# Optimization experiments

Measured on AMD Instinct MI355X. Metric: run time of the kernel, lower is better.

## Reference

```python
import jax, jax.numpy as jnp
import numpy as np

NUM_HEADS = 16


def setup_inputs() -> dict:
    key = jax.random.key(0)
    ks = jax.random.split(key, 4)
    B, C, T, D = 1, 1, 3072, 1024
    s = 1.0 / np.sqrt(D)
    return {
        "x": jax.random.normal(ks[0], (B, C, T, D), dtype=jnp.float32),
        "Wq": jax.random.normal(ks[1], (D, D), dtype=jnp.float32) * s,
        "bq": jnp.zeros((D,), dtype=jnp.float32),
        "Wk": jax.random.normal(ks[2], (D, D), dtype=jnp.float32) * s,
        "bk": jnp.zeros((D,), dtype=jnp.float32),
        "Wv": jax.random.normal(ks[3], (D, D), dtype=jnp.float32) * s,
        "bv": jnp.zeros((D,), dtype=jnp.float32),
        "gamma": jnp.float32(0.5),  # learned scalar; 0.0 at torch init, nonzero here for a meaningful signal
    }


def reference(x, Wq, bq, Wk, bk, Wv, bv, gamma):
    # x: (B, C, T, D); Linear acts on last dim (torch: y = x @ W.T + b)
    B, C, T, D = x.shape
    H = NUM_HEADS
    q = (jnp.einsum("bctd,ed->bcte", x, Wq) + bq).reshape(B, -1, T, H)  # (B, X, T, H), X = C*D/H
    k = (jnp.einsum("bctd,ed->bcte", x, Wk) + bk).reshape(B, -1, T, H)
    v = (jnp.einsum("bctd,ed->bcte", x, Wv) + bv).reshape(B, -1, T, H)
    q = q.transpose(0, 3, 2, 1)  # (B, H, T, X)
    k = k.transpose(0, 3, 1, 2)  # (B, H, X, T)
    energy = q @ k               # (B, H, T, T)  -- note: NO 1/sqrt(d) scaling, as in source
    attn = jax.nn.softmax(energy, axis=-1)
    v = v.transpose(0, 3, 2, 1)  # (B, H, T, X)
    out = attn @ v               # (B, H, T, X)
    out = out.transpose(0, 2, 3, 1).reshape(B, T, -1)  # (B, T, X*H) = (B, T, C*D)
    # residual broadcast: (B, T, C*D) + (B, C, T, D); valid since B == C == 1
    return gamma * out + x
```

## Files before the change

### kernel.cpp

```cpp
#include <hip/hip_runtime.h>


typedef _Float16 v8h __attribute__((ext_vector_type(8)));
typedef _Float16 v4h __attribute__((ext_vector_type(4)));
typedef float    v4f __attribute__((ext_vector_type(4)));

#define TSEQ 3072
#define DM   1024
#define NH   16
#define XD   64
#define LOG2E 1.44269504f

__device__ __forceinline__ void async_load16(const void* g, void* l) {
  __builtin_amdgcn_global_load_lds(
      (const __attribute__((address_space(1))) unsigned int*)g,
      (__attribute__((address_space(3))) unsigned int*)l,
      16, 0, 0);
}

__device__ __forceinline__ float fexp2(float x) {
  float r; asm("v_exp_f32 %0, %1" : "=v"(r) : "v"(x)); return r;
}

extern "C" __global__ __launch_bounds__(256) void cvt_kernel(
    const float* __restrict__ x, const float* __restrict__ wq,
    const float* __restrict__ wk, const float* __restrict__ wv,
    _Float16* __restrict__ xb, _Float16* __restrict__ wb)
{
  const int NX4 = (TSEQ * DM) / 4;
  const int NT  = NX4 * 2;
  for (int i = blockIdx.x * blockDim.x + threadIdx.x; i < NT;
       i += gridDim.x * blockDim.x) {
    float4 v;
    _Float16* dst;
    if (i < NX4) {
      v = ((const float4*)x)[i];
      dst = xb + (size_t)i * 4;
    } else {
      const int j = i - NX4;
      const int n = j >> 8;
      if (n < 1024)      v = ((const float4*)wq)[j];
      else if (n < 2048) v = ((const float4*)wk)[j - 262144];
      else               v = ((const float4*)wv)[j - 524288];
      dst = wb + (size_t)j * 4;
    }
    v4h h;
    h[0] = (_Float16)v.x; h[1] = (_Float16)v.y;
    h[2] = (_Float16)v.z; h[3] = (_Float16)v.w;
    *(v4h*)dst = h;
  }
}

extern "C" __global__ __launch_bounds__(256) void qkv_gemm_kernel(
    const _Float16* __restrict__ xb, const _Float16* __restrict__ wb,
    const float* __restrict__ bq, const float* __restrict__ bk,
    const float* __restrict__ bv,
    _Float16* __restrict__ qlin, _Float16* __restrict__ klin,
    _Float16* __restrict__ vlin)
{
  __shared__ _Float16 As[128 * 32];
  __shared__ _Float16 Bs[128 * 32];
  const int tid = threadIdx.x;
  const int w = tid >> 6, l = tid & 63;
  const int li = l & 15, lg = l >> 4;
  const int wm = w >> 1, wn = w & 1;
  const int bid = blockIdx.x;
  const int swz = (bid & 7) * 72 + (bid >> 3);
  const int m0 = (swz / 24) * 128, n0 = (swz % 24) * 128;
  v4f acc[4][4] = {};
  const int srow = l >> 2;
  const int scol = (l & 3) * 8;
  for (int k0 = 0; k0 < DM; k0 += 32) {
#pragma unroll
    for (int c = 0; c < 2; ++c) {
      const int rbase = c * 64 + w * 16;
      async_load16(xb + (size_t)(m0 + rbase + srow) * DM + k0 + scol, &As[rbase * 32]);
      async_load16(wb + (size_t)(n0 + rbase + srow) * DM + k0 + scol, &Bs[rbase * 32]);
    }
    __syncthreads();
    v8h af[4], bf[4];
#pragma unroll
    for (int mi = 0; mi < 4; ++mi)
      af[mi] = *(const v8h*)&As[(wm * 64 + mi * 16 + li) * 32 + lg * 8];
#pragma unroll
    for (int ni = 0; ni < 4; ++ni)
      bf[ni] = *(const v8h*)&Bs[(wn * 64 + ni * 16 + li) * 32 + lg * 8];
#pragma unroll
    for (int mi = 0; mi < 4; ++mi)
#pragma unroll
      for (int ni = 0; ni < 4; ++ni)
        acc[mi][ni] = __builtin_amdgcn_mfma_f32_16x16x32_f16(
            af[mi], bf[ni], acc[mi][ni], 0, 0, 0);
    __syncthreads();
  }
  const int which = n0 >> 10;
  const int ebase = n0 & 1023;
  const float* bias = which == 0 ? bq : (which == 1 ? bk : bv);
  _Float16* outp = which == 0 ? qlin : (which == 1 ? klin : vlin);
#pragma unroll
  for (int mi = 0; mi < 4; ++mi)
#pragma unroll
    for (int r = 0; r < 4; ++r) {
      const int t = m0 + wm * 64 + mi * 16 + lg * 4 + r;
#pragma unroll
      for (int ni = 0; ni < 4; ++ni) {
        const int e = ebase + wn * 64 + ni * 16 + li;
        outp[(size_t)t * DM + e] = (_Float16)(acc[mi][ni][r] + bias[e]);
      }
    }
}

extern "C" __global__ __launch_bounds__(256) void repack_kernel(
    const _Float16* __restrict__ qlin, const _Float16* __restrict__ klin,
    const _Float16* __restrict__ vlin,
    _Float16* __restrict__ qh, _Float16* __restrict__ kh,
    _Float16* __restrict__ vt)
{
  const int NE = NH * TSEQ * XD;
  for (int g = blockIdx.x * blockDim.x + threadIdx.x; g < 3 * NE;
       g += gridDim.x * blockDim.x) {
    if (g < 2 * NE) {
      const int gg = (g < NE) ? g : g - NE;
      const int xx = gg & 63;
      const int rest = gg >> 6;
      const int h = rest / TSEQ;
      const int i = rest - h * TSEQ;
      const int t = xx * 48 + (i >> 6);
      const int e = ((i & 63) << 4) + h;
      if (g < NE) qh[gg] = qlin[t * DM + e];
      else        kh[gg] = (_Float16)((float)klin[t * DM + e] * LOG2E);
    } else {
      const int o = g - 2 * NE;
      const int j = o % TSEQ;
      const int rest = o / TSEQ;
      const int xx = rest & 63;
      const int h = rest >> 6;
      const int t = xx * 48 + (j >> 6);
      const int e = ((j & 63) << 4) + h;
      vt[o] = vlin[t * DM + e];
    }
  }
}

extern "C" __global__ __launch_bounds__(256) void attn_kernel(
    const _Float16* __restrict__ qh, const _Float16* __restrict__ kh,
    const _Float16* __restrict__ vt, _Float16* __restrict__ pOut)
{
  __shared__ _Float16 Ks[64 * 64];
  __shared__ _Float16 Vs[64 * 64];
  const int tid = threadIdx.x;
  const int w = tid >> 6, l = tid & 63;
  const int li = l & 15, lg = l >> 4;
  const int head = blockIdx.y;
  const int i0 = blockIdx.x * 64;
  const size_t hb = (size_t)head * TSEQ * XD;

  v8h qf0, qf1;
  {
    const _Float16* qrow = qh + hb + (size_t)(i0 + w * 16 + li) * XD;
    qf0 = *(const v8h*)(qrow + lg * 8);
    qf1 = *(const v8h*)(qrow + 32 + lg * 8);
  }
  float m2 = 24.0f * LOG2E;
  float l4 = 0.0f;
  v4f oacc[4] = {};
  const int r8 = l >> 3, c8 = l & 7;

  for (int j0 = 0; j0 < TSEQ; j0 += 64) {
#pragma unroll
    for (int s = 0; s < 2; ++s) {
      const int n = w * 2 + s;
      const int row = n * 8 + r8;
      async_load16(kh + hb + (size_t)(j0 + row) * XD + ((c8 ^ (row & 7)) * 8),
                   Ks + n * 512);
      async_load16(vt + hb + (size_t)row * TSEQ + j0 + ((c8 ^ (row & 7)) * 8),
                   Vs + n * 512);
    }
    __syncthreads();

    v4f e4[4];
#pragma unroll
    for (int kt = 0; kt < 4; ++kt) {
      const int krow = kt * 16 + li;
      const v8h kf0 = *(const v8h*)&Ks[krow * 64 + ((lg ^ (krow & 7)) * 8)];
      const v8h kf1 = *(const v8h*)&Ks[krow * 64 + (((4 + lg) ^ (krow & 7)) * 8)];
      v4f a = {};
      a = __builtin_amdgcn_mfma_f32_16x16x32_f16(kf0, qf0, a, 0, 0, 0);
      a = __builtin_amdgcn_mfma_f32_16x16x32_f16(kf1, qf1, a, 0, 0, 0);
      e4[kt] = a;
    }

    float p[4][4];
#pragma unroll
    for (int kt = 0; kt < 4; ++kt)
#pragma unroll
      for (int r = 0; r < 4; ++r) p[kt][r] = fexp2(e4[kt][r] - m2);

    float lmax = fmaxf(fmaxf(fmaxf(e4[0][0], e4[0][1]), fmaxf(e4[0][2], e4[0][3])),
                       fmaxf(fmaxf(e4[1][0], e4[1][1]), fmaxf(e4[1][2], e4[1][3])));
    lmax = fmaxf(lmax,
           fmaxf(fmaxf(fmaxf(e4[2][0], e4[2][1]), fmaxf(e4[2][2], e4[2][3])),
                 fmaxf(fmaxf(e4[3][0], e4[3][1]), fmaxf(e4[3][2], e4[3][3]))));
    if (__any(lmax > m2 + 11.5f)) {
      float rm = lmax;
      rm = fmaxf(rm, __shfl_xor(rm, 16, 64));
      rm = fmaxf(rm, __shfl_xor(rm, 32, 64));
      const float fs = (rm > m2) ? fexp2(m2 - rm) : 1.0f;
#pragma unroll
      for (int kt = 0; kt < 4; ++kt)
#pragma unroll
        for (int r = 0; r < 4; ++r) p[kt][r] *= fs;
      l4 *= fs;
#pragma unroll
      for (int mi = 0; mi < 4; ++mi) oacc[mi] *= fs;
      m2 = fmaxf(m2, rm);
    }

    v4h pv[4];
#pragma unroll
    for (int kt = 0; kt < 4; ++kt)
#pragma unroll
      for (int r = 0; r < 4; ++r) pv[kt][r] = (_Float16)p[kt][r];
    l4 += ((p[0][0] + p[0][1]) + (p[0][2] + p[0][3]))
        + ((p[1][0] + p[1][1]) + (p[1][2] + p[1][3]))
        + ((p[2][0] + p[2][1]) + (p[2][2] + p[2][3]))
        + ((p[3][0] + p[3][1]) + (p[3][2] + p[3][3]));

#pragma unroll
    for (int mi = 0; mi < 4; ++mi) {
      const int vrow = mi * 16 + li;
      const int vb = vrow * 64 + (lg & 1) * 4;
      v4f a = oacc[mi];
#pragma unroll
      for (int kt = 0; kt < 4; ++kt) {
        const v4h vf = *(const v4h*)&Vs[vb + (((kt * 2 + (lg >> 1)) ^ (vrow & 7)) * 8)];
        a = __builtin_amdgcn_mfma_f32_16x16x16f16(vf, pv[kt], a, 0, 0, 0);
      }
      oacc[mi] = a;
    }
    __syncthreads();
  }

  float ls = l4;
  ls += __shfl_xor(ls, 16, 64);
  ls += __shfl_xor(ls, 32, 64);
  const float inv = 1.0f / ls;
  const int irow = i0 + w * 16 + li;
#pragma unroll
  for (int mi = 0; mi < 4; ++mi) {
    v4h o4;
#pragma unroll
    for (int r = 0; r < 4; ++r) o4[r] = (_Float16)(oacc[mi][r] * inv);
    *(v4h*)&pOut[(size_t)irow * DM + head * 64 + mi * 16 + lg * 4] = o4;
  }
}

extern "C" __global__ __launch_bounds__(256) void epilogue_kernel(
    const _Float16* __restrict__ pO, const float* __restrict__ xin,
    const float* __restrict__ gscal, float* __restrict__ outp)
{
  __shared__ _Float16 po[8 * 1024];
  const int tid = threadIdx.x;
  const size_t t0 = (size_t)blockIdx.x * 8;
  {
    const _Float16* src = pO + t0 * DM + tid * 32;
    v8h* d = (v8h*)&po[tid * 32];
#pragma unroll
    for (int c = 0; c < 4; ++c) d[c] = *(const v8h*)(src + c * 8);
  }
  __syncthreads();
  const float g = gscal[0];
  const int tr = tid >> 5;
  const int d0 = (tid & 31) * 32;
  const size_t rb = (t0 + tr) * DM + d0;
#pragma unroll
  for (int c4 = 0; c4 < 8; ++c4) {
    const float4 xi = *(const float4*)&xin[rb + c4 * 4];
    float4 r;
    r.x = g * (float)po[tr * 1024 + ((c4 * 4 + 0) & 15) * 64 + ((d0 + c4 * 4 + 0) >> 4)] + xi.x;
    r.y = g * (float)po[tr * 1024 + ((c4 * 4 + 1) & 15) * 64 + ((d0 + c4 * 4 + 1) >> 4)] + xi.y;
    r.z = g * (float)po[tr * 1024 + ((c4 * 4 + 2) & 15) * 64 + ((d0 + c4 * 4 + 2) >> 4)] + xi.z;
    r.w = g * (float)po[tr * 1024 + ((c4 * 4 + 3) & 15) * 64 + ((d0 + c4 * 4 + 3) >> 4)] + xi.w;
    *(float4*)&outp[rb + c4 * 4] = r;
  }
}

extern "C" void kernel_launch(void* const* d_in, const int* in_sizes, int n_in,
                              void* d_out, int out_size, void* d_ws, size_t ws_size,
                              hipStream_t stream)
{
  const float* x  = (const float*)d_in[0];
  const float* Wq = (const float*)d_in[1];
  const float* bq = (const float*)d_in[2];
  const float* Wk = (const float*)d_in[3];
  const float* bk = (const float*)d_in[4];
  const float* Wv = (const float*)d_in[5];
  const float* bv = (const float*)d_in[6];
  const float* gm = (const float*)d_in[7];
  float* outp = (float*)d_out;
  char* ws = (char*)d_ws;
  const size_t SZH = (size_t)TSEQ * DM * sizeof(_Float16);
  _Float16* xb   = (_Float16*)(ws);
  _Float16* wb   = (_Float16*)(ws + SZH);
  _Float16* qlin = (_Float16*)(ws + 2 * SZH);
  _Float16* klin = (_Float16*)(ws + 3 * SZH);
  _Float16* vlin = (_Float16*)(ws + 4 * SZH);
  _Float16* qhp  = (_Float16*)(ws + 5 * SZH);
  _Float16* khp  = (_Float16*)(ws + 6 * SZH);
  _Float16* vtp  = (_Float16*)(ws + 7 * SZH);
  _Float16* pO   = (_Float16*)(ws);

  cvt_kernel<<<dim3(1024), dim3(256), 0, stream>>>(x, Wq, Wk, Wv, xb, wb);
  qkv_gemm_kernel<<<dim3(576), dim3(256), 0, stream>>>(xb, wb, bq, bk, bv,
                                                       qlin, klin, vlin);
  repack_kernel<<<dim3(4096), dim3(256), 0, stream>>>(qlin, klin, vlin,
                                                      qhp, khp, vtp);
  attn_kernel<<<dim3(48, 16), dim3(256), 0, stream>>>(qhp, khp, vtp, pO);
  epilogue_kernel<<<dim3(384), dim3(256), 0, stream>>>(pO, x, gm, outp);
  (void)in_sizes; (void)n_in; (void)out_size; (void)ws_size;
}
```

Baseline: 152.7 us.

## Split attention key range across two wave groups with log-sum-exp merge

The attention block grows to 512 threads. Two groups of four waves each handle alternating 64-key tiles of the sequence for the same 64 query rows, so per-block parallelism doubles, which matters because the grid has only 768 blocks. At the end the partial outputs are merged through LDS using each group's log-sum-exp weights. The change also uses packed round-toward-zero f16 conversion for P, reorganises the max reduction into 3-input max calls, and simplifies the swizzle index. The costs are double the LDS footprint, an extra barrier with a merge step, and slightly different rounding of P.

```diff
diff --git a/kernel.cpp b/kernel.cpp
--- a/kernel.cpp
+++ b/kernel.cpp
@@ -3,6 +3,8 @@
 
 typedef _Float16 v8h __attribute__((ext_vector_type(8)));
 typedef _Float16 v4h __attribute__((ext_vector_type(4)));
+typedef __fp16   v2pk __attribute__((ext_vector_type(2)));
+typedef __fp16   v4pk __attribute__((ext_vector_type(4)));
 typedef float    v4f __attribute__((ext_vector_type(4)));
 
 #define TSEQ 3072
@@ -20,6 +22,12 @@
 
 __device__ __forceinline__ float fexp2(float x) {
   float r; asm("v_exp_f32 %0, %1" : "=v"(r) : "v"(x)); return r;
+}
+__device__ __forceinline__ float flog2(float x) {
+  float r; asm("v_log_f32 %0, %1" : "=v"(r) : "v"(x)); return r;
+}
+__device__ __forceinline__ float fmax3(float a, float b, float c) {
+  return fmaxf(fmaxf(a, b), c);
 }
 
 extern "C" __global__ __launch_bounds__(256) void cvt_kernel(
@@ -142,22 +150,24 @@
   }
 }
 
-extern "C" __global__ __launch_bounds__(256) void attn_kernel(
+extern "C" __global__ __launch_bounds__(512) void attn_kernel(
     const _Float16* __restrict__ qh, const _Float16* __restrict__ kh,
     const _Float16* __restrict__ vt, _Float16* __restrict__ pOut)
 {
-  __shared__ _Float16 Ks[64 * 64];
-  __shared__ _Float16 Vs[64 * 64];
+  __shared__ _Float16 Ks[2][64 * 64];
+  __shared__ _Float16 Vs[2][64 * 64];
+  __shared__ float sml[4][16];
   const int tid = threadIdx.x;
   const int w = tid >> 6, l = tid & 63;
   const int li = l & 15, lg = l >> 4;
+  const int wq = w & 3, g = w >> 2;
   const int head = blockIdx.y;
   const int i0 = blockIdx.x * 64;
   const size_t hb = (size_t)head * TSEQ * XD;
 
   v8h qf0, qf1;
   {
-    const _Float16* qrow = qh + hb + (size_t)(i0 + w * 16 + li) * XD;
+    const _Float16* qrow = qh + hb + (size_t)(i0 + wq * 16 + li) * XD;
     qf0 = *(const v8h*)(qrow + lg * 8);
     qf1 = *(const v8h*)(qrow + 32 + lg * 8);
   }
@@ -166,15 +176,16 @@
   v4f oacc[4] = {};
   const int r8 = l >> 3, c8 = l & 7;
 
-  for (int j0 = 0; j0 < TSEQ; j0 += 64) {
+  for (int j0 = 0; j0 < TSEQ; j0 += 128) {
+    const int jt = j0 + g * 64;
 #pragma unroll
     for (int s = 0; s < 2; ++s) {
-      const int n = w * 2 + s;
+      const int n = wq * 2 + s;
       const int row = n * 8 + r8;
-      async_load16(kh + hb + (size_t)(j0 + row) * XD + ((c8 ^ (row & 7)) * 8),
-                   Ks + n * 512);
-      async_load16(vt + hb + (size_t)row * TSEQ + j0 + ((c8 ^ (row & 7)) * 8),
-                   Vs + n * 512);
+      async_load16(kh + hb + (size_t)(jt + row) * XD + ((c8 ^ (row & 7)) * 8),
+                   &Ks[g][n * 512]);
+      async_load16(vt + hb + (size_t)row * TSEQ + jt + ((c8 ^ (row & 7)) * 8),
+                   &Vs[g][n * 512]);
     }
     __syncthreads();
 
@@ -182,8 +193,8 @@
 #pragma unroll
     for (int kt = 0; kt < 4; ++kt) {
       const int krow = kt * 16 + li;
-      const v8h kf0 = *(const v8h*)&Ks[krow * 64 + ((lg ^ (krow & 7)) * 8)];
-      const v8h kf1 = *(const v8h*)&Ks[krow * 64 + (((4 + lg) ^ (krow & 7)) * 8)];
+      const v8h kf0 = *(const v8h*)&Ks[g][krow * 64 + ((lg ^ (li & 7)) * 8)];
+      const v8h kf1 = *(const v8h*)&Ks[g][krow * 64 + (((4 + lg) ^ (li & 7)) * 8)];
       v4f a = {};
       a = __builtin_amdgcn_mfma_f32_16x16x32_f16(kf0, qf0, a, 0, 0, 0);
       a = __builtin_amdgcn_mfma_f32_16x16x32_f16(kf1, qf1, a, 0, 0, 0);
@@ -196,11 +207,12 @@
 #pragma unroll
       for (int r = 0; r < 4; ++r) p[kt][r] = fexp2(e4[kt][r] - m2);
 
-    float lmax = fmaxf(fmaxf(fmaxf(e4[0][0], e4[0][1]), fmaxf(e4[0][2], e4[0][3])),
-                       fmaxf(fmaxf(e4[1][0], e4[1][1]), fmaxf(e4[1][2], e4[1][3])));
-    lmax = fmaxf(lmax,
-           fmaxf(fmaxf(fmaxf(e4[2][0], e4[2][1]), fmaxf(e4[2][2], e4[2][3])),
-                 fmaxf(fmaxf(e4[3][0], e4[3][1]), fmaxf(e4[3][2], e4[3][3]))));
+    const float lmax = fmax3(
+        fmax3(fmax3(e4[0][0], e4[0][1], e4[0][2]),
+              fmax3(e4[0][3], e4[1][0], e4[1][1]),
+              fmax3(e4[1][2], e4[1][3], e4[2][0])),
+        fmax3(e4[2][1], e4[2][2], e4[2][3]),
+        fmax3(e4[3][0], fmaxf(e4[3][1], e4[3][2]), e4[3][3]));
     if (__any(lmax > m2 + 11.5f)) {
       float rm = lmax;
       rm = fmaxf(rm, __shfl_xor(rm, 16, 64));
@@ -218,9 +230,12 @@
 
     v4h pv[4];
 #pragma unroll
-    for (int kt = 0; kt < 4; ++kt)
-#pragma unroll
-      for (int r = 0; r < 4; ++r) pv[kt][r] = (_Float16)p[kt][r];
+    for (int kt = 0; kt < 4; ++kt) {
+      const v2pk lo = __builtin_amdgcn_cvt_pkrtz(p[kt][0], p[kt][1]);
+      const v2pk hi = __builtin_amdgcn_cvt_pkrtz(p[kt][2], p[kt][3]);
+      const v4pk pk = __builtin_shufflevector(lo, hi, 0, 1, 2, 3);
+      pv[kt] = __builtin_bit_cast(v4h, pk);
+    }
     l4 += ((p[0][0] + p[0][1]) + (p[0][2] + p[0][3]))
         + ((p[1][0] + p[1][1]) + (p[1][2] + p[1][3]))
         + ((p[2][0] + p[2][1]) + (p[2][2] + p[2][3]))
@@ -233,7 +248,7 @@
       v4f a = oacc[mi];
 #pragma unroll
       for (int kt = 0; kt < 4; ++kt) {
-        const v4h vf = *(const v4h*)&Vs[vb + (((kt * 2 + (lg >> 1)) ^ (vrow & 7)) * 8)];
+        const v4h vf = *(const v4h*)&Vs[g][vb + (((kt * 2 + (lg >> 1)) ^ (li & 7)) * 8)];
         a = __builtin_amdgcn_mfma_f32_16x16x16f16(vf, pv[kt], a, 0, 0, 0);
       }
       oacc[mi] = a;
@@ -245,13 +260,35 @@
   ls += __shfl_xor(ls, 16, 64);
   ls += __shfl_xor(ls, 32, 64);
   const float inv = 1.0f / ls;
-  const int irow = i0 + w * 16 + li;
-#pragma unroll
-  for (int mi = 0; mi < 4; ++mi) {
-    v4h o4;
-#pragma unroll
-    for (int r = 0; r < 4; ++r) o4[r] = (_Float16)(oacc[mi][r] * inv);
-    *(v4h*)&pOut[(size_t)irow * DM + head * 64 + mi * 16 + lg * 4] = o4;
+  const float s = m2 + flog2(ls);
+  _Float16* mb = &Ks[0][0];
+  if (g == 1) {
+    if (lg == 0) sml[wq][li] = s;
+#pragma unroll
+    for (int mi = 0; mi < 4; ++mi) {
+      v4h o4;
+#pragma unroll
+      for (int r = 0; r < 4; ++r) o4[r] = (_Float16)(oacc[mi][r] * inv);
+      *(v4h*)&mb[wq * 1024 + li * 64 + mi * 16 + lg * 4] = o4;
+    }
+  }
+  __syncthreads();
+  if (g == 0) {
+    const float s1 = sml[wq][li];
+    const float M = fmaxf(s, s1);
+    const float u0 = fexp2(s - M), u1 = fexp2(s1 - M);
+    const float den = 1.0f / (u0 + u1);
+    const float c0 = u0 * den * inv, c1 = u1 * den;
+    const int irow = i0 + wq * 16 + li;
+#pragma unroll
+    for (int mi = 0; mi < 4; ++mi) {
+      const v4h o1 = *(const v4h*)&mb[wq * 1024 + li * 64 + mi * 16 + lg * 4];
+      v4h o4;
+#pragma unroll
+      for (int r = 0; r < 4; ++r)
+        o4[r] = (_Float16)(c0 * oacc[mi][r] + c1 * (float)o1[r]);
+      *(v4h*)&pOut[(size_t)irow * DM + head * 64 + mi * 16 + lg * 4] = o4;
+    }
   }
 }
 
@@ -315,7 +352,7 @@
                                                        qlin, klin, vlin);
   repack_kernel<<<dim3(4096), dim3(256), 0, stream>>>(qlin, klin, vlin,
                                                       qhp, khp, vtp);
-  attn_kernel<<<dim3(48, 16), dim3(256), 0, stream>>>(qhp, khp, vtp, pO);
+  attn_kernel<<<dim3(48, 16), dim3(512), 0, stream>>>(qhp, khp, vtp, pO);
   epilogue_kernel<<<dim3(384), dim3(256), 0, stream>>>(pO, x, gm, outp);
   (void)in_sizes; (void)n_in; (void)out_size; (void)ws_size;
 }
```

Result: no change. 155.0 us (+1.5%).
